# Kernel tuning notes

Measured on AMD Instinct MI355X. Metric: run time of the kernel, lower is better.

## Reference

```python
import jax, jax.numpy as jnp
import numpy as np

# config (matches init_kwargs)
D, H, KV, HD, L, F, V, NC, S = 1024, 16, 4, 64, 6, 4096, 4096, 15, 16
KVD = KV * HD            # 256
ATTN_SCALING = 1.0
EPS = 1e-6
POS = 7                  # current cache write position


def _rms(x, w):
    return x * jax.lax.rsqrt(jnp.mean(x * x, axis=-1, keepdims=True) + EPS) * w


def _rot(x):
    h = x.shape[-1] // 2
    return jnp.concatenate([-x[..., h:], x[..., :h]], axis=-1)


def setup_inputs() -> dict:
    key = jax.random.key(0)
    ks = iter(jax.random.split(key, 24))
    def rn(shape, s):
        return jax.random.normal(next(ks), shape, jnp.float32) * s
    return {
        "input_embeds": rn((1, D, 1, 1), 1.0),
        "cache_length": POS,
        "key_cache": rn((1, L * KVD, 1, S), 0.5),
        "key_padding_mask": jnp.where(jnp.arange(S) <= POS, 0.0, -1e9)[None, :].astype(jnp.float32),
        "kv_cache_update_mask": (jnp.arange(S) == POS).astype(jnp.float32)[None, :],
        "value_cache": rn((1, L * KVD, 1, S), 0.5),
        "inv_freq": 1.0 / (10000.0 ** (jnp.arange(0, HD, 2, dtype=jnp.float32) / HD)),
        "Wq": rn((L, H * HD, D), 0.02),
        "Wk": rn((L, KVD, D), 0.02),
        "Wv": rn((L, KVD, D), 0.02),
        "Wo": rn((L, D, H * HD), 0.02),
        "ln1_w": jnp.ones((L, D), jnp.float32),
        "ln2_w": jnp.ones((L, D), jnp.float32),
        "qn_w": jnp.ones((L, HD), jnp.float32),
        "kn_w": jnp.ones((L, HD), jnp.float32),
        "Wgate": rn((L, F, D), 0.02),
        "Wup": rn((L, F, D), 0.02),
        "Wdown": rn((L, D, F), 0.02),
        "norm_w": jnp.ones((D,), jnp.float32),
        "lm_head_w": rn((NC, V, D), 0.02),
    }


def _forward(input_embeds, key_cache, key_padding_mask, kv_cache_update_mask,
             value_cache, inv_freq, Wq, Wk, Wv, Wo, ln1_w, ln2_w, qn_w, kn_w,
             Wgate, Wup, Wdown, norm_w, lm_head_w, cache_length):
    pos = jnp.asarray(cache_length, jnp.float32)
    freqs = inv_freq * pos                       # [HD/2]
    emb = jnp.concatenate([freqs, freqs])        # [HD]
    cos = jnp.cos(emb) * ATTN_SCALING
    sin = jnp.sin(emb) * ATTN_SCALING
    umask = kv_cache_update_mask[0]              # [S]
    pmask = key_padding_mask[0]                  # [S]
    kcache = key_cache.reshape(L, KVD, S)
    vcache = value_cache.reshape(L, KVD, S)
    hidden0 = input_embeds.reshape(D)
    n_rep = H // KV
    scale = 1.0 / (HD ** 0.5)

    def layer(hidden, p):
        Wq_, Wk_, Wv_, Wo_, ln1, ln2, qn, kn, Wg_, Wu_, Wd_, kc_l, vc_l = p
        h = _rms(hidden, ln1)
        q = _rms((Wq_ @ h).reshape(H, HD), qn)   # [H,HD]
        k = _rms((Wk_ @ h).reshape(KV, HD), kn)  # [KV,HD]
        v = (Wv_ @ h).reshape(KV, HD)
        q = q * cos + _rot(q) * sin
        k = k * cos + _rot(k) * sin
        nk = k.reshape(KVD)
        nv = v.reshape(KVD)
        # masked scatter-write into this layer's cache slice
        kc = kc_l * (1.0 - umask) + nk[:, None] * umask   # [KVD,S]
        vc = vc_l * (1.0 - umask) + nv[:, None] * umask
        kc = jnp.repeat(kc.reshape(KV, HD, S), n_rep, axis=0)  # GQA expand -> [H,HD,S]
        vc = jnp.repeat(vc.reshape(KV, HD, S), n_rep, axis=0)
        scores = jnp.einsum('hd,hds->hs', q, kc) * scale + pmask  # [H,S]
        aw = jax.nn.softmax(scores, axis=-1)
        ao = jnp.einsum('hs,hds->hd', aw, vc).reshape(H * HD)
        hidden = hidden + Wo_ @ ao
        h = _rms(hidden, ln2)
        hidden = hidden + Wd_ @ (jax.nn.silu(Wg_ @ h) * (Wu_ @ h))
        return hidden, (nk, nv)

    hidden, (nks, nvs) = jax.lax.scan(
        layer, hidden0,
        (Wq, Wk, Wv, Wo, ln1_w, ln2_w, qn_w, kn_w, Wgate, Wup, Wdown, kcache, vcache))

    normed = _rms(hidden, norm_w)                          # [D]
    all_logits = jnp.einsum('nvd,d->nv', lm_head_w, normed)[None]  # [1,NC,V]
    hidden_out = normed.reshape(1, D, 1, 1)
    um4 = kv_cache_update_mask[:, None, None, :]           # [1,1,1,S]
    new_k = nks.reshape(1, L * KVD, 1, 1)
    new_v = nvs.reshape(1, L * KVD, 1, 1)
    nkc = key_cache * (1.0 - um4) + new_k * um4
    nvc = value_cache * (1.0 - um4) + new_v * um4
    return (all_logits, hidden_out, nkc, nvc)


def reference(input_embeds, cache_length, key_cache, key_padding_mask,
              kv_cache_update_mask, value_cache, inv_freq, Wq, Wk, Wv, Wo,
              ln1_w, ln2_w, qn_w, kn_w, Wgate, Wup, Wdown, norm_w, lm_head_w):
    return _forward(input_embeds, key_cache, key_padding_mask, kv_cache_update_mask,
                    value_cache, inv_freq, Wq, Wk, Wv, Wo, ln1_w, ln2_w, qn_w, kn_w,
                    Wgate, Wup, Wdown, norm_w, lm_head_w, cache_length)
```

## Files before the change

### kernel.cpp

```cpp
#include <hip/hip_runtime.h>

#define DD     1024
#define HH     16
#define KVH    4
#define HDIM   64
#define NLAYER 6
#define FDIM   4096
#define VDIM   4096
#define NCODE  15
#define SS     16
#define KVDIM  256
#define EPSF   1e-6f

__device__ __forceinline__ float dot4(float4 a, float4 b){
  return a.x*b.x + a.y*b.y + a.z*b.z + a.w*b.w;
}
__device__ __forceinline__ float wave_sum(float v){
  #pragma unroll
  for (int o=32;o;o>>=1) v += __shfl_xor(v,o);
  return v;
}
__device__ __forceinline__ float grp16_sum(float v){
  #pragma unroll
  for (int o=8;o;o>>=1) v += __shfl_xor(v,o);
  return v;
}
__device__ __forceinline__ float grp16_max(float v){
  #pragma unroll
  for (int o=8;o;o>>=1) v = fmaxf(v, __shfl_xor(v,o));
  return v;
}

__global__ __launch_bounds__(256) void k_init(const float* __restrict__ emb,
                                              float* __restrict__ hidden){
  ((float4*)hidden)[threadIdx.x] = ((const float4*)emb)[threadIdx.x];
}

__global__ __launch_bounds__(256) void k_qkv(
    const float* __restrict__ Wq, const float* __restrict__ Wk, const float* __restrict__ Wv,
    const float* __restrict__ hidden, const float* __restrict__ ln,
    float* __restrict__ out )
{
  __shared__ float xs[DD];
  __shared__ float red[4];
  const int t = threadIdx.x, lane = t & 63, wid = t >> 6;
  float4 hv = ((const float4*)hidden)[t];
  float ss = wave_sum(dot4(hv,hv));
  if (lane==0) red[wid] = ss;
  __syncthreads();
  const float inv = rsqrtf((red[0]+red[1]+red[2]+red[3])*(1.0f/DD) + EPSF);
  float4 lw = ((const float4*)ln)[t];
  float4 xv; xv.x=hv.x*inv*lw.x; xv.y=hv.y*inv*lw.y; xv.z=hv.z*inv*lw.z; xv.w=hv.w*inv*lw.w;
  ((float4*)xs)[t] = xv;
  __syncthreads();
  const int row = blockIdx.x*4 + wid;
  const float* Wrow;
  if (row < 1024)      Wrow = Wq + (size_t)row*DD;
  else if (row < 1280) Wrow = Wk + (size_t)(row-1024)*DD;
  else                 Wrow = Wv + (size_t)(row-1280)*DD;
  const float4* w4 = (const float4*)Wrow;
  const float4* x4 = (const float4*)xs;
  float acc = 0.f;
  #pragma unroll
  for (int j=0;j<4;j++) acc += dot4(w4[j*64+lane], x4[j*64+lane]);
  acc = wave_sum(acc);
  if (lane==0) out[row] = acc;
}

__global__ __launch_bounds__(256) void k_attn(
    const float* __restrict__ qbuf, const float* __restrict__ kbuf, const float* __restrict__ vbuf,
    const float* __restrict__ qn, const float* __restrict__ kn,
    const float* __restrict__ inv_freq, const int* __restrict__ cache_len,
    const float* __restrict__ kcache_l, const float* __restrict__ vcache_l,
    const float* __restrict__ pmask, const float* __restrict__ umask,
    float* __restrict__ ao, float* __restrict__ knew, float* __restrict__ vnew)
{
  __shared__ float qsh[DD];
  __shared__ float ksh[KVDIM];
  __shared__ float vsh[KVDIM];
  __shared__ float awsh[HH*SS];
  __shared__ float umsh[SS], pmsh[SS];
  const int t = threadIdx.x;
  if (t < SS){ umsh[t]=umask[t]; pmsh[t]=pmask[t]; }
  const float pos = (float)cache_len[0];

  {
    const int idx16 = t & 15;
    float4 q = ((const float4*)qbuf)[t];
    float ss = grp16_sum(dot4(q,q));
    const float inv = rsqrtf(ss*(1.0f/HDIM)+EPSF);
    float4 w = ((const float4*)qn)[idx16];
    float x0=q.x*inv*w.x, x1=q.y*inv*w.y, x2=q.z*inv*w.z, x3=q.w*inv*w.w;
    float p0=__shfl_xor(x0,8), p1=__shfl_xor(x1,8), p2=__shfl_xor(x2,8), p3=__shfl_xor(x3,8);
    const int d0 = idx16*4;
    const bool lolane = (idx16 < 8);
    const int m = lolane ? d0 : d0-32;
    const float f0=inv_freq[m]*pos, f1=inv_freq[m+1]*pos, f2=inv_freq[m+2]*pos, f3=inv_freq[m+3]*pos;
    const float sgn = lolane ? -1.f : 1.f;
    float4 r;
    r.x = x0*cosf(f0) + sgn*p0*sinf(f0);
    r.y = x1*cosf(f1) + sgn*p1*sinf(f1);
    r.z = x2*cosf(f2) + sgn*p2*sinf(f2);
    r.w = x3*cosf(f3) + sgn*p3*sinf(f3);
    ((float4*)qsh)[t] = r;
  }
  if (t < 64){
    const int idx16 = t & 15;
    float4 k = ((const float4*)kbuf)[t];
    float ss = grp16_sum(dot4(k,k));
    const float inv = rsqrtf(ss*(1.0f/HDIM)+EPSF);
    float4 w = ((const float4*)kn)[idx16];
    float x0=k.x*inv*w.x, x1=k.y*inv*w.y, x2=k.z*inv*w.z, x3=k.w*inv*w.w;
    float p0=__shfl_xor(x0,8), p1=__shfl_xor(x1,8), p2=__shfl_xor(x2,8), p3=__shfl_xor(x3,8);
    const int d0 = idx16*4;
    const bool lolane = (idx16 < 8);
    const int m = lolane ? d0 : d0-32;
    const float f0=inv_freq[m]*pos, f1=inv_freq[m+1]*pos, f2=inv_freq[m+2]*pos, f3=inv_freq[m+3]*pos;
    const float sgn = lolane ? -1.f : 1.f;
    float4 r;
    r.x = x0*cosf(f0) + sgn*p0*sinf(f0);
    r.y = x1*cosf(f1) + sgn*p1*sinf(f1);
    r.z = x2*cosf(f2) + sgn*p2*sinf(f2);
    r.w = x3*cosf(f3) + sgn*p3*sinf(f3);
    ((float4*)ksh)[t] = r;
    ((float4*)knew)[t] = r;
    float4 v = ((const float4*)vbuf)[t];
    ((float4*)vsh)[t] = v;
    ((float4*)vnew)[t] = v;
  }
  __syncthreads();
  {
    const int h = t>>4, s = t&15, kvh = h>>2;
    const float um = umsh[s], pm = pmsh[s];
    const float* kcol = kcache_l + (size_t)(kvh*HDIM)*SS + s;
    const float* ksrc = ksh + kvh*HDIM;
    const float* qv   = qsh + h*HDIM;
    float dot = 0.f;
    #pragma unroll
    for (int d=0; d<HDIM; d++){
      float kc = kcol[d*SS]*(1.f-um) + ksrc[d]*um;
      dot += qv[d]*kc;
    }
    const float sc = dot*0.125f + pm;
    const float mx = grp16_max(sc);
    const float e  = expf(sc-mx);
    const float sm = grp16_sum(e);
    awsh[t] = e/sm;
  }
  __syncthreads();
  {
    const int h = t>>4, idx16 = t&15, kvh = h>>2;
    const int cb = kvh*HDIM + idx16*4;
    float a0=0,a1=0,a2=0,a3=0;
    #pragma unroll
    for (int s=0;s<SS;s++){
      const float aw = awsh[h*16+s];
      const float um = umsh[s];
      a0 += aw*(vcache_l[(size_t)(cb+0)*SS+s]*(1.f-um)+vsh[cb+0]*um);
      a1 += aw*(vcache_l[(size_t)(cb+1)*SS+s]*(1.f-um)+vsh[cb+1]*um);
      a2 += aw*(vcache_l[(size_t)(cb+2)*SS+s]*(1.f-um)+vsh[cb+2]*um);
      a3 += aw*(vcache_l[(size_t)(cb+3)*SS+s]*(1.f-um)+vsh[cb+3]*um);
    }
    ((float4*)ao)[t] = make_float4(a0,a1,a2,a3);
  }
}

__global__ __launch_bounds__(256) void k_o(
    const float* __restrict__ Wo, const float* __restrict__ ao, float* __restrict__ hidden)
{
  __shared__ float xs[DD];
  const int t=threadIdx.x, lane=t&63, wid=t>>6;
  ((float4*)xs)[t] = ((const float4*)ao)[t];
  __syncthreads();
  const int row = blockIdx.x*4 + wid;
  const float4* w4 = (const float4*)(Wo + (size_t)row*DD);
  const float4* x4 = (const float4*)xs;
  float acc=0.f;
  #pragma unroll
  for (int j=0;j<4;j++) acc += dot4(w4[j*64+lane], x4[j*64+lane]);
  acc = wave_sum(acc);
  if (lane==0) hidden[row] += acc;
}

__global__ __launch_bounds__(256) void k_gu(
    const float* __restrict__ Wg, const float* __restrict__ Wu,
    const float* __restrict__ hidden, const float* __restrict__ ln,
    float* __restrict__ act)
{
  __shared__ float xs[DD];
  __shared__ float red[4];
  const int t=threadIdx.x, lane=t&63, wid=t>>6;
  float4 hv = ((const float4*)hidden)[t];
  float ss = wave_sum(dot4(hv,hv));
  if (lane==0) red[wid]=ss;
  __syncthreads();
  const float inv = rsqrtf((red[0]+red[1]+red[2]+red[3])*(1.0f/DD) + EPSF);
  float4 lw = ((const float4*)ln)[t];
  float4 xv; xv.x=hv.x*inv*lw.x; xv.y=hv.y*inv*lw.y; xv.z=hv.z*inv*lw.z; xv.w=hv.w*inv*lw.w;
  ((float4*)xs)[t] = xv;
  __syncthreads();
  const int row = blockIdx.x*4 + wid;
  const float4* g4 = (const float4*)(Wg + (size_t)row*DD);
  const float4* u4 = (const float4*)(Wu + (size_t)row*DD);
  const float4* x4 = (const float4*)xs;
  float ag=0.f, au=0.f;
  #pragma unroll
  for (int j=0;j<4;j++){
    float4 x = x4[j*64+lane];
    ag += dot4(g4[j*64+lane], x);
    au += dot4(u4[j*64+lane], x);
  }
  ag = wave_sum(ag); au = wave_sum(au);
  if (lane==0){
    float sg = ag/(1.f+expf(-ag));
    act[row] = sg*au;
  }
}

__global__ __launch_bounds__(256) void k_down(
    const float* __restrict__ Wd, const float* __restrict__ act, float* __restrict__ hidden)
{
  __shared__ float xs[FDIM];
  const int t=threadIdx.x, lane=t&63, wid=t>>6;
  #pragma unroll
  for (int j=0;j<4;j++) ((float4*)xs)[j*256+t] = ((const float4*)act)[j*256+t];
  __syncthreads();
  const int row = blockIdx.x*4 + wid;
  const float4* w4 = (const float4*)(Wd + (size_t)row*FDIM);
  const float4* x4 = (const float4*)xs;
  float acc=0.f;
  #pragma unroll
  for (int j=0;j<16;j++) acc += dot4(w4[j*64+lane], x4[j*64+lane]);
  acc = wave_sum(acc);
  if (lane==0) hidden[row] += acc;
}

__global__ __launch_bounds__(256) void k_finalize(
    const float* __restrict__ hidden, const float* __restrict__ norm_w,
    const float* __restrict__ kcache, const float* __restrict__ vcache,
    const float* __restrict__ knew, const float* __restrict__ vnew,
    const float* __restrict__ umask,
    float* __restrict__ normed, float* __restrict__ out_hidden,
    float* __restrict__ out_nkc, float* __restrict__ out_nvc)
{
  if (blockIdx.x == 0){
    __shared__ float red[4];
    const int t=threadIdx.x, lane=t&63, wid=t>>6;
    float4 hv = ((const float4*)hidden)[t];
    float ss = wave_sum(dot4(hv,hv));
    if (lane==0) red[wid]=ss;
    __syncthreads();
    const float inv = rsqrtf((red[0]+red[1]+red[2]+red[3])*(1.0f/DD) + EPSF);
    float4 w = ((const float4*)norm_w)[t];
    float4 nv; nv.x=hv.x*inv*w.x; nv.y=hv.y*inv*w.y; nv.z=hv.z*inv*w.z; nv.w=hv.w*inv*w.w;
    ((float4*)normed)[t]   = nv;
    ((float4*)out_hidden)[t] = nv;
  } else {
    const int j = (blockIdx.x-1)*256 + threadIdx.x;
    if (j < NLAYER*KVDIM*SS){
      const int s = j & 15, c = j >> 4;
      const float um = umask[s];
      out_nkc[j] = kcache[j]*(1.f-um) + knew[c]*um;
    } else {
      const int i = j - NLAYER*KVDIM*SS;
      const int s = i & 15, c = i >> 4;
      const float um = umask[s];
      out_nvc[i] = vcache[i]*(1.f-um) + vnew[c]*um;
    }
  }
}

__global__ __launch_bounds__(256) void k_lmhead(
    const float* __restrict__ W, const float* __restrict__ normed, float* __restrict__ out)
{
  __shared__ float xs[DD];
  const int t=threadIdx.x, lane=t&63, wid=t>>6;
  ((float4*)xs)[t] = ((const float4*)normed)[t];
  __syncthreads();
  const int row = blockIdx.x*4 + wid;
  const float4* w4 = (const float4*)(W + (size_t)row*DD);
  const float4* x4 = (const float4*)xs;
  float acc=0.f;
  #pragma unroll
  for (int j=0;j<4;j++) acc += dot4(w4[j*64+lane], x4[j*64+lane]);
  acc = wave_sum(acc);
  if (lane==0) out[row] = acc;
}

extern "C" void kernel_launch(void* const* d_in, const int* in_sizes, int n_in,
                              void* d_out, int out_size, void* d_ws, size_t ws_size,
                              hipStream_t stream)
{
  const float* emb    = (const float*)d_in[0];
  const int*   clen   = (const int*)  d_in[1];
  const float* kcache = (const float*)d_in[2];
  const float* pmask  = (const float*)d_in[3];
  const float* umask  = (const float*)d_in[4];
  const float* vcache = (const float*)d_in[5];
  const float* invf   = (const float*)d_in[6];
  const float* Wq     = (const float*)d_in[7];
  const float* Wk     = (const float*)d_in[8];
  const float* Wv     = (const float*)d_in[9];
  const float* Wo     = (const float*)d_in[10];
  const float* ln1    = (const float*)d_in[11];
  const float* ln2    = (const float*)d_in[12];
  const float* qn     = (const float*)d_in[13];
  const float* kn     = (const float*)d_in[14];
  const float* Wg     = (const float*)d_in[15];
  const float* Wu     = (const float*)d_in[16];
  const float* Wd     = (const float*)d_in[17];
  const float* nw     = (const float*)d_in[18];
  const float* lmw    = (const float*)d_in[19];
  float* out = (float*)d_out;
  float* ws  = (float*)d_ws;

  float* hidden = ws;
  float* qkv    = ws + 1024;
  float* ao     = ws + 2560;
  float* act    = ws + 3584;
  float* knew   = ws + 7680;
  float* vnew   = ws + 9216;
  float* normed = ws + 10752;

  float* out_logits = out;
  float* out_hidden = out + NCODE*VDIM;
  float* out_nkc    = out_hidden + DD;
  float* out_nvc    = out_nkc + NLAYER*KVDIM*SS;

  k_init<<<1,256,0,stream>>>(emb, hidden);
  for (int l=0; l<NLAYER; l++){
    k_qkv<<<384,256,0,stream>>>(Wq + (size_t)l*HH*HDIM*DD, Wk + (size_t)l*KVDIM*DD,
                                Wv + (size_t)l*KVDIM*DD, hidden, ln1 + l*DD, qkv);
    k_attn<<<1,256,0,stream>>>(qkv, qkv+1024, qkv+1280, qn + l*HDIM, kn + l*HDIM,
                               invf, clen,
                               kcache + (size_t)l*KVDIM*SS, vcache + (size_t)l*KVDIM*SS,
                               pmask, umask, ao, knew + l*KVDIM, vnew + l*KVDIM);
    k_o<<<256,256,0,stream>>>(Wo + (size_t)l*DD*HH*HDIM, ao, hidden);
    k_gu<<<1024,256,0,stream>>>(Wg + (size_t)l*FDIM*DD, Wu + (size_t)l*FDIM*DD,
                                hidden, ln2 + l*DD, act);
    k_down<<<256,256,0,stream>>>(Wd + (size_t)l*DD*FDIM, act, hidden);
  }
  k_finalize<<<193,256,0,stream>>>(hidden, nw, kcache, vcache, knew, vnew, umask,
                                   normed, out_hidden, out_nkc, out_nvc);
  k_lmhead<<<15360,256,0,stream>>>(lmw, normed, out_logits);
}
```

Baseline: 678.7 us.

## Fuse whole decode step into one persistent kernel with grid barriers

Replaces the roughly 32 separate kernel launches (qkv, attention, o-proj, gate/up, down per layer, plus finalize and lm head) with a single persistent 256-block kernel. A software grid barrier built on atomics separates the phases. The tiny attention step is computed redundantly in every block, which removes the single-block attention launch and the separate ao buffer. Cos/sin are precomputed once, and the gate/up, down and lm-head loops load several weight rows per wave to raise memory-level parallelism. The risks are barrier spin cost, the requirement that all 256 blocks be co-resident, and running the bandwidth-bound lm head with fewer blocks.

```diff
diff --git a/kernel.cpp b/kernel.cpp
--- a/kernel.cpp
+++ b/kernel.cpp
@@ -11,6 +11,7 @@
 #define SS     16
 #define KVDIM  256
 #define EPSF   1e-6f
+#define NBLK   256
 
 __device__ __forceinline__ float dot4(float4 a, float4 b){
   return a.x*b.x + a.y*b.y + a.z*b.z + a.w*b.w;
@@ -31,260 +32,298 @@
   return v;
 }
 
-__global__ __launch_bounds__(256) void k_init(const float* __restrict__ emb,
-                                              float* __restrict__ hidden){
-  ((float4*)hidden)[threadIdx.x] = ((const float4*)emb)[threadIdx.x];
-}
-
-__global__ __launch_bounds__(256) void k_qkv(
-    const float* __restrict__ Wq, const float* __restrict__ Wk, const float* __restrict__ Wv,
-    const float* __restrict__ hidden, const float* __restrict__ ln,
-    float* __restrict__ out )
+__device__ __forceinline__ void gbar(unsigned* bar){
+  __syncthreads();
+  if (threadIdx.x == 0){
+    __threadfence();
+    unsigned g = __hip_atomic_load(bar+1, __ATOMIC_RELAXED, __HIP_MEMORY_SCOPE_AGENT);
+    unsigned a = __hip_atomic_fetch_add(bar, 1u, __ATOMIC_RELAXED, __HIP_MEMORY_SCOPE_AGENT);
+    if (a == (unsigned)(NBLK-1)){
+      __hip_atomic_store(bar, 0u, __ATOMIC_RELAXED, __HIP_MEMORY_SCOPE_AGENT);
+      __hip_atomic_fetch_add(bar+1, 1u, __ATOMIC_RELEASE, __HIP_MEMORY_SCOPE_AGENT);
+    } else {
+      while (__hip_atomic_load(bar+1, __ATOMIC_RELAXED, __HIP_MEMORY_SCOPE_AGENT) == g)
+        __builtin_amdgcn_s_sleep(2);
+    }
+    __threadfence();
+  }
+  __syncthreads();
+}
+
+__global__ void k_barinit(unsigned* bar){ bar[0]=0u; bar[1]=0u; }
+
+__device__ __forceinline__ float4 rms_rope16(float4 x, const float4* nw4,
+                                             const float* cosb, const float* sinb,
+                                             int idx16)
 {
-  __shared__ float xs[DD];
-  __shared__ float red[4];
+  float ssum = grp16_sum(dot4(x,x));
+  const float inv = rsqrtf(ssum*(1.0f/HDIM)+EPSF);
+  float4 w = nw4[idx16];
+  float x0=x.x*inv*w.x, x1=x.y*inv*w.y, x2=x.z*inv*w.z, x3=x.w*inv*w.w;
+  float p0=__shfl_xor(x0,8), p1=__shfl_xor(x1,8), p2=__shfl_xor(x2,8), p3=__shfl_xor(x3,8);
+  float4 c = ((const float4*)cosb)[idx16];
+  float4 s = ((const float4*)sinb)[idx16];
+  const float sgn = (idx16 < 8) ? -1.f : 1.f;
+  float4 r;
+  r.x = x0*c.x + sgn*p0*s.x;
+  r.y = x1*c.y + sgn*p1*s.y;
+  r.z = x2*c.z + sgn*p2*s.z;
+  r.w = x3*c.w + sgn*p3*s.w;
+  return r;
+}
+
+__global__ __launch_bounds__(256) void k_fused(
+    const float* __restrict__ emb,   const int* __restrict__ clen,
+    const float* __restrict__ kcache,const float* __restrict__ pmask,
+    const float* __restrict__ umask, const float* __restrict__ vcache,
+    const float* __restrict__ invf,
+    const float* __restrict__ Wq,    const float* __restrict__ Wk,
+    const float* __restrict__ Wv,    const float* __restrict__ Wo,
+    const float* __restrict__ ln1,   const float* __restrict__ ln2,
+    const float* __restrict__ qn,    const float* __restrict__ kn,
+    const float* __restrict__ Wg,    const float* __restrict__ Wu,
+    const float* __restrict__ Wd,    const float* __restrict__ nw,
+    const float* __restrict__ lmw,
+    float* __restrict__ out_logits,  float* __restrict__ out_hidden,
+    float* __restrict__ out_nkc,     float* __restrict__ out_nvc,
+    float* __restrict__ ws,          unsigned* __restrict__ bar)
+{
   const int t = threadIdx.x, lane = t & 63, wid = t >> 6;
-  float4 hv = ((const float4*)hidden)[t];
-  float ss = wave_sum(dot4(hv,hv));
-  if (lane==0) red[wid] = ss;
-  __syncthreads();
-  const float inv = rsqrtf((red[0]+red[1]+red[2]+red[3])*(1.0f/DD) + EPSF);
-  float4 lw = ((const float4*)ln)[t];
-  float4 xv; xv.x=hv.x*inv*lw.x; xv.y=hv.y*inv*lw.y; xv.z=hv.z*inv*lw.z; xv.w=hv.w*inv*lw.w;
-  ((float4*)xs)[t] = xv;
-  __syncthreads();
-  const int row = blockIdx.x*4 + wid;
-  const float* Wrow;
-  if (row < 1024)      Wrow = Wq + (size_t)row*DD;
-  else if (row < 1280) Wrow = Wk + (size_t)(row-1024)*DD;
-  else                 Wrow = Wv + (size_t)(row-1280)*DD;
-  const float4* w4 = (const float4*)Wrow;
-  const float4* x4 = (const float4*)xs;
-  float acc = 0.f;
-  #pragma unroll
-  for (int j=0;j<4;j++) acc += dot4(w4[j*64+lane], x4[j*64+lane]);
-  acc = wave_sum(acc);
-  if (lane==0) out[row] = acc;
-}
-
-__global__ __launch_bounds__(256) void k_attn(
-    const float* __restrict__ qbuf, const float* __restrict__ kbuf, const float* __restrict__ vbuf,
-    const float* __restrict__ qn, const float* __restrict__ kn,
-    const float* __restrict__ inv_freq, const int* __restrict__ cache_len,
-    const float* __restrict__ kcache_l, const float* __restrict__ vcache_l,
-    const float* __restrict__ pmask, const float* __restrict__ umask,
-    float* __restrict__ ao, float* __restrict__ knew, float* __restrict__ vnew)
-{
-  __shared__ float qsh[DD];
-  __shared__ float ksh[KVDIM];
-  __shared__ float vsh[KVDIM];
+  const int gw = blockIdx.x*4 + wid;
+
+  __shared__ float xs[FDIM];
+  __shared__ float ksh[KVDIM], vsh[KVDIM];
   __shared__ float awsh[HH*SS];
   __shared__ float umsh[SS], pmsh[SS];
-  const int t = threadIdx.x;
-  if (t < SS){ umsh[t]=umask[t]; pmsh[t]=pmask[t]; }
-  const float pos = (float)cache_len[0];
+  __shared__ float red[4];
+
+  float* hidden = ws;
+  float* qkv    = ws + 1024;
+  float* act    = ws + 2560;
+  float* knew   = ws + 6656;
+  float* vnew   = ws + 8192;
+  float* cosb   = ws + 9728;
+  float* sinb   = ws + 9792;
+
+  if (t < SS){ umsh[t] = umask[t]; pmsh[t] = pmask[t]; }
+
+  if (blockIdx.x == 0){
+    ((float4*)hidden)[t] = ((const float4*)emb)[t];
+    if (t < 64){
+      const float f = invf[t & 31] * (float)clen[0];
+      cosb[t] = cosf(f);
+      sinb[t] = sinf(f);
+    }
+  }
+  gbar(bar);
+
+  for (int l = 0; l < NLAYER; ++l){
+    const float* Wq_l = Wq + (size_t)l*HH*HDIM*DD;
+    const float* Wk_l = Wk + (size_t)l*KVDIM*DD;
+    const float* Wv_l = Wv + (size_t)l*KVDIM*DD;
+    const float* Wo_l = Wo + (size_t)l*DD*HH*HDIM;
+    const float* Wg_l = Wg + (size_t)l*FDIM*DD;
+    const float* Wu_l = Wu + (size_t)l*FDIM*DD;
+    const float* Wd_l = Wd + (size_t)l*DD*FDIM;
+    const float* kc_l = kcache + (size_t)l*KVDIM*SS;
+    const float* vc_l = vcache + (size_t)l*KVDIM*SS;
+
+    {
+      float4 hv = ((const float4*)hidden)[t];
+      float ssum = wave_sum(dot4(hv,hv));
+      if (lane==0) red[wid] = ssum;
+      __syncthreads();
+      const float inv = rsqrtf((red[0]+red[1]+red[2]+red[3])*(1.0f/DD) + EPSF);
+      float4 lw = ((const float4*)(ln1 + l*DD))[t];
+      float4 xv; xv.x=hv.x*inv*lw.x; xv.y=hv.y*inv*lw.y; xv.z=hv.z*inv*lw.z; xv.w=hv.w*inv*lw.w;
+      ((float4*)xs)[t] = xv;
+      __syncthreads();
+      const float4* x4 = (const float4*)xs;
+      const float4* wa = (const float4*)(Wq_l + (size_t)gw*DD);
+      if (gw < 512){
+        const float* Wrow = (gw < 256) ? (Wk_l + (size_t)gw*DD) : (Wv_l + (size_t)(gw-256)*DD);
+        const float4* wb = (const float4*)Wrow;
+        float4 a0=wa[lane], a1=wa[64+lane], a2=wa[128+lane], a3=wa[192+lane];
+        float4 b0=wb[lane], b1=wb[64+lane], b2=wb[128+lane], b3=wb[192+lane];
+        float accA = dot4(a0,x4[lane])+dot4(a1,x4[64+lane])+dot4(a2,x4[128+lane])+dot4(a3,x4[192+lane]);
+        float accB = dot4(b0,x4[lane])+dot4(b1,x4[64+lane])+dot4(b2,x4[128+lane])+dot4(b3,x4[192+lane]);
+        accA = wave_sum(accA); accB = wave_sum(accB);
+        if (lane==0){ qkv[gw] = accA; qkv[1024+gw] = accB; }
+      } else {
+        float4 a0=wa[lane], a1=wa[64+lane], a2=wa[128+lane], a3=wa[192+lane];
+        float accA = dot4(a0,x4[lane])+dot4(a1,x4[64+lane])+dot4(a2,x4[128+lane])+dot4(a3,x4[192+lane]);
+        accA = wave_sum(accA);
+        if (lane==0) qkv[gw] = accA;
+      }
+    }
+    gbar(bar);
+
+    {
+      const int idx16 = t & 15;
+      {
+        float4 q = ((const float4*)qkv)[t];
+        float4 r = rms_rope16(q, (const float4*)(qn + l*HDIM), cosb, sinb, idx16);
+        ((float4*)xs)[t] = r;
+      }
+      if (t < 64){
+        float4 k = ((const float4*)(qkv+1024))[t];
+        float4 r = rms_rope16(k, (const float4*)(kn + l*HDIM), cosb, sinb, idx16);
+        ((float4*)ksh)[t] = r;
+        float4 v = ((const float4*)(qkv+1280))[t];
+        ((float4*)vsh)[t] = v;
+        if (blockIdx.x == 0){
+          ((float4*)(knew + l*KVDIM))[t] = r;
+          ((float4*)(vnew + l*KVDIM))[t] = v;
+        }
+      }
+      __syncthreads();
+      {
+        const int h = t>>4, s = t&15, kvh = h>>2;
+        const float um = umsh[s], pm = pmsh[s];
+        const float* kcol = kc_l + (size_t)(kvh*HDIM)*SS + s;
+        const float* ksrc = ksh + kvh*HDIM;
+        const float* qv   = xs + h*HDIM;
+        float dot = 0.f;
+        #pragma unroll
+        for (int d=0; d<HDIM; d++){
+          float kc = kcol[d*SS]*(1.f-um) + ksrc[d]*um;
+          dot += qv[d]*kc;
+        }
+        const float sc = dot*0.125f + pm;
+        const float mx = grp16_max(sc);
+        const float e  = expf(sc-mx);
+        const float sm = grp16_sum(e);
+        awsh[t] = e/sm;
+      }
+      __syncthreads();
+      {
+        const int h = t>>4, i16 = t&15, kvh = h>>2;
+        const int cb = kvh*HDIM + i16*4;
+        float a0=0,a1=0,a2=0,a3=0;
+        #pragma unroll
+        for (int s=0;s<SS;s++){
+          const float aw = awsh[h*16+s];
+          const float um = umsh[s];
+          a0 += aw*(vc_l[(size_t)(cb+0)*SS+s]*(1.f-um)+vsh[cb+0]*um);
+          a1 += aw*(vc_l[(size_t)(cb+1)*SS+s]*(1.f-um)+vsh[cb+1]*um);
+          a2 += aw*(vc_l[(size_t)(cb+2)*SS+s]*(1.f-um)+vsh[cb+2]*um);
+          a3 += aw*(vc_l[(size_t)(cb+3)*SS+s]*(1.f-um)+vsh[cb+3]*um);
+        }
+        ((float4*)(xs+1024))[t] = make_float4(a0,a1,a2,a3);
+      }
+      __syncthreads();
+      {
+        const float4* w4 = (const float4*)(Wo_l + (size_t)gw*DD);
+        const float4* x4 = (const float4*)(xs+1024);
+        float4 w0=w4[lane], w1=w4[64+lane], w2=w4[128+lane], w3=w4[192+lane];
+        float acc = dot4(w0,x4[lane])+dot4(w1,x4[64+lane])+dot4(w2,x4[128+lane])+dot4(w3,x4[192+lane]);
+        acc = wave_sum(acc);
+        if (lane==0) hidden[gw] += acc;
+      }
+    }
+    gbar(bar);
+
+    {
+      float4 hv = ((const float4*)hidden)[t];
+      float ssum = wave_sum(dot4(hv,hv));
+      if (lane==0) red[wid] = ssum;
+      __syncthreads();
+      const float inv = rsqrtf((red[0]+red[1]+red[2]+red[3])*(1.0f/DD) + EPSF);
+      float4 lw = ((const float4*)(ln2 + l*DD))[t];
+      float4 xv; xv.x=hv.x*inv*lw.x; xv.y=hv.y*inv*lw.y; xv.z=hv.z*inv*lw.z; xv.w=hv.w*inv*lw.w;
+      ((float4*)xs)[t] = xv;
+      __syncthreads();
+      const float4* x4 = (const float4*)xs;
+      #pragma unroll
+      for (int half=0; half<2; half++){
+        const int r0 = gw + half*2048;
+        const int r1 = r0 + 1024;
+        const float4* g0 = (const float4*)(Wg_l + (size_t)r0*DD);
+        const float4* u0 = (const float4*)(Wu_l + (size_t)r0*DD);
+        const float4* g1 = (const float4*)(Wg_l + (size_t)r1*DD);
+        const float4* u1 = (const float4*)(Wu_l + (size_t)r1*DD);
+        float4 wg0[4], wu0[4], wg1[4], wu1[4];
+        #pragma unroll
+        for (int j=0;j<4;j++){
+          wg0[j]=g0[j*64+lane]; wu0[j]=u0[j*64+lane];
+          wg1[j]=g1[j*64+lane]; wu1[j]=u1[j*64+lane];
+        }
+        float ag0=0,au0=0,ag1=0,au1=0;
+        #pragma unroll
+        for (int j=0;j<4;j++){
+          float4 x = x4[j*64+lane];
+          ag0+=dot4(wg0[j],x); au0+=dot4(wu0[j],x);
+          ag1+=dot4(wg1[j],x); au1+=dot4(wu1[j],x);
+        }
+        ag0=wave_sum(ag0); au0=wave_sum(au0); ag1=wave_sum(ag1); au1=wave_sum(au1);
+        if (lane==0){
+          act[r0] = ag0/(1.f+expf(-ag0))*au0;
+          act[r1] = ag1/(1.f+expf(-ag1))*au1;
+        }
+      }
+    }
+    gbar(bar);
+
+    {
+      #pragma unroll
+      for (int j=0;j<4;j++) ((float4*)xs)[j*256+t] = ((const float4*)act)[j*256+t];
+      __syncthreads();
+      const float4* w4 = (const float4*)(Wd_l + (size_t)gw*FDIM);
+      const float4* x4 = (const float4*)xs;
+      float4 wv[16];
+      #pragma unroll
+      for (int j=0;j<16;j++) wv[j] = w4[j*64+lane];
+      float acc = 0.f;
+      #pragma unroll
+      for (int j=0;j<16;j++) acc += dot4(wv[j], x4[j*64+lane]);
+      acc = wave_sum(acc);
+      if (lane==0) hidden[gw] += acc;
+    }
+    gbar(bar);
+  }
 
   {
-    const int idx16 = t & 15;
-    float4 q = ((const float4*)qbuf)[t];
-    float ss = grp16_sum(dot4(q,q));
-    const float inv = rsqrtf(ss*(1.0f/HDIM)+EPSF);
-    float4 w = ((const float4*)qn)[idx16];
-    float x0=q.x*inv*w.x, x1=q.y*inv*w.y, x2=q.z*inv*w.z, x3=q.w*inv*w.w;
-    float p0=__shfl_xor(x0,8), p1=__shfl_xor(x1,8), p2=__shfl_xor(x2,8), p3=__shfl_xor(x3,8);
-    const int d0 = idx16*4;
-    const bool lolane = (idx16 < 8);
-    const int m = lolane ? d0 : d0-32;
-    const float f0=inv_freq[m]*pos, f1=inv_freq[m+1]*pos, f2=inv_freq[m+2]*pos, f3=inv_freq[m+3]*pos;
-    const float sgn = lolane ? -1.f : 1.f;
-    float4 r;
-    r.x = x0*cosf(f0) + sgn*p0*sinf(f0);
-    r.y = x1*cosf(f1) + sgn*p1*sinf(f1);
-    r.z = x2*cosf(f2) + sgn*p2*sinf(f2);
-    r.w = x3*cosf(f3) + sgn*p3*sinf(f3);
-    ((float4*)qsh)[t] = r;
-  }
-  if (t < 64){
-    const int idx16 = t & 15;
-    float4 k = ((const float4*)kbuf)[t];
-    float ss = grp16_sum(dot4(k,k));
-    const float inv = rsqrtf(ss*(1.0f/HDIM)+EPSF);
-    float4 w = ((const float4*)kn)[idx16];
-    float x0=k.x*inv*w.x, x1=k.y*inv*w.y, x2=k.z*inv*w.z, x3=k.w*inv*w.w;
-    float p0=__shfl_xor(x0,8), p1=__shfl_xor(x1,8), p2=__shfl_xor(x2,8), p3=__shfl_xor(x3,8);
-    const int d0 = idx16*4;
-    const bool lolane = (idx16 < 8);
-    const int m = lolane ? d0 : d0-32;
-    const float f0=inv_freq[m]*pos, f1=inv_freq[m+1]*pos, f2=inv_freq[m+2]*pos, f3=inv_freq[m+3]*pos;
-    const float sgn = lolane ? -1.f : 1.f;
-    float4 r;
-    r.x = x0*cosf(f0) + sgn*p0*sinf(f0);
-    r.y = x1*cosf(f1) + sgn*p1*sinf(f1);
-    r.z = x2*cosf(f2) + sgn*p2*sinf(f2);
-    r.w = x3*cosf(f3) + sgn*p3*sinf(f3);
-    ((float4*)ksh)[t] = r;
-    ((float4*)knew)[t] = r;
-    float4 v = ((const float4*)vbuf)[t];
-    ((float4*)vsh)[t] = v;
-    ((float4*)vnew)[t] = v;
-  }
-  __syncthreads();
-  {
-    const int h = t>>4, s = t&15, kvh = h>>2;
-    const float um = umsh[s], pm = pmsh[s];
-    const float* kcol = kcache_l + (size_t)(kvh*HDIM)*SS + s;
-    const float* ksrc = ksh + kvh*HDIM;
-    const float* qv   = qsh + h*HDIM;
-    float dot = 0.f;
-    #pragma unroll
-    for (int d=0; d<HDIM; d++){
-      float kc = kcol[d*SS]*(1.f-um) + ksrc[d]*um;
-      dot += qv[d]*kc;
-    }
-    const float sc = dot*0.125f + pm;
-    const float mx = grp16_max(sc);
-    const float e  = expf(sc-mx);
-    const float sm = grp16_sum(e);
-    awsh[t] = e/sm;
-  }
-  __syncthreads();
-  {
-    const int h = t>>4, idx16 = t&15, kvh = h>>2;
-    const int cb = kvh*HDIM + idx16*4;
-    float a0=0,a1=0,a2=0,a3=0;
-    #pragma unroll
-    for (int s=0;s<SS;s++){
-      const float aw = awsh[h*16+s];
-      const float um = umsh[s];
-      a0 += aw*(vcache_l[(size_t)(cb+0)*SS+s]*(1.f-um)+vsh[cb+0]*um);
-      a1 += aw*(vcache_l[(size_t)(cb+1)*SS+s]*(1.f-um)+vsh[cb+1]*um);
-      a2 += aw*(vcache_l[(size_t)(cb+2)*SS+s]*(1.f-um)+vsh[cb+2]*um);
-      a3 += aw*(vcache_l[(size_t)(cb+3)*SS+s]*(1.f-um)+vsh[cb+3]*um);
-    }
-    ((float4*)ao)[t] = make_float4(a0,a1,a2,a3);
-  }
-}
-
-__global__ __launch_bounds__(256) void k_o(
-    const float* __restrict__ Wo, const float* __restrict__ ao, float* __restrict__ hidden)
-{
-  __shared__ float xs[DD];
-  const int t=threadIdx.x, lane=t&63, wid=t>>6;
-  ((float4*)xs)[t] = ((const float4*)ao)[t];
-  __syncthreads();
-  const int row = blockIdx.x*4 + wid;
-  const float4* w4 = (const float4*)(Wo + (size_t)row*DD);
-  const float4* x4 = (const float4*)xs;
-  float acc=0.f;
-  #pragma unroll
-  for (int j=0;j<4;j++) acc += dot4(w4[j*64+lane], x4[j*64+lane]);
-  acc = wave_sum(acc);
-  if (lane==0) hidden[row] += acc;
-}
-
-__global__ __launch_bounds__(256) void k_gu(
-    const float* __restrict__ Wg, const float* __restrict__ Wu,
-    const float* __restrict__ hidden, const float* __restrict__ ln,
-    float* __restrict__ act)
-{
-  __shared__ float xs[DD];
-  __shared__ float red[4];
-  const int t=threadIdx.x, lane=t&63, wid=t>>6;
-  float4 hv = ((const float4*)hidden)[t];
-  float ss = wave_sum(dot4(hv,hv));
-  if (lane==0) red[wid]=ss;
-  __syncthreads();
-  const float inv = rsqrtf((red[0]+red[1]+red[2]+red[3])*(1.0f/DD) + EPSF);
-  float4 lw = ((const float4*)ln)[t];
-  float4 xv; xv.x=hv.x*inv*lw.x; xv.y=hv.y*inv*lw.y; xv.z=hv.z*inv*lw.z; xv.w=hv.w*inv*lw.w;
-  ((float4*)xs)[t] = xv;
-  __syncthreads();
-  const int row = blockIdx.x*4 + wid;
-  const float4* g4 = (const float4*)(Wg + (size_t)row*DD);
-  const float4* u4 = (const float4*)(Wu + (size_t)row*DD);
-  const float4* x4 = (const float4*)xs;
-  float ag=0.f, au=0.f;
-  #pragma unroll
-  for (int j=0;j<4;j++){
-    float4 x = x4[j*64+lane];
-    ag += dot4(g4[j*64+lane], x);
-    au += dot4(u4[j*64+lane], x);
-  }
-  ag = wave_sum(ag); au = wave_sum(au);
-  if (lane==0){
-    float sg = ag/(1.f+expf(-ag));
-    act[row] = sg*au;
-  }
-}
-
-__global__ __launch_bounds__(256) void k_down(
-    const float* __restrict__ Wd, const float* __restrict__ act, float* __restrict__ hidden)
-{
-  __shared__ float xs[FDIM];
-  const int t=threadIdx.x, lane=t&63, wid=t>>6;
-  #pragma unroll
-  for (int j=0;j<4;j++) ((float4*)xs)[j*256+t] = ((const float4*)act)[j*256+t];
-  __syncthreads();
-  const int row = blockIdx.x*4 + wid;
-  const float4* w4 = (const float4*)(Wd + (size_t)row*FDIM);
-  const float4* x4 = (const float4*)xs;
-  float acc=0.f;
-  #pragma unroll
-  for (int j=0;j<16;j++) acc += dot4(w4[j*64+lane], x4[j*64+lane]);
-  acc = wave_sum(acc);
-  if (lane==0) hidden[row] += acc;
-}
-
-__global__ __launch_bounds__(256) void k_finalize(
-    const float* __restrict__ hidden, const float* __restrict__ norm_w,
-    const float* __restrict__ kcache, const float* __restrict__ vcache,
-    const float* __restrict__ knew, const float* __restrict__ vnew,
-    const float* __restrict__ umask,
-    float* __restrict__ normed, float* __restrict__ out_hidden,
-    float* __restrict__ out_nkc, float* __restrict__ out_nvc)
-{
-  if (blockIdx.x == 0){
-    __shared__ float red[4];
-    const int t=threadIdx.x, lane=t&63, wid=t>>6;
     float4 hv = ((const float4*)hidden)[t];
-    float ss = wave_sum(dot4(hv,hv));
-    if (lane==0) red[wid]=ss;
+    float ssum = wave_sum(dot4(hv,hv));
+    if (lane==0) red[wid] = ssum;
     __syncthreads();
     const float inv = rsqrtf((red[0]+red[1]+red[2]+red[3])*(1.0f/DD) + EPSF);
-    float4 w = ((const float4*)norm_w)[t];
+    float4 w = ((const float4*)nw)[t];
     float4 nv; nv.x=hv.x*inv*w.x; nv.y=hv.y*inv*w.y; nv.z=hv.z*inv*w.z; nv.w=hv.w*inv*w.w;
-    ((float4*)normed)[t]   = nv;
-    ((float4*)out_hidden)[t] = nv;
-  } else {
-    const int j = (blockIdx.x-1)*256 + threadIdx.x;
-    if (j < NLAYER*KVDIM*SS){
+    ((float4*)xs)[t] = nv;
+    if (blockIdx.x == 0) ((float4*)out_hidden)[t] = nv;
+    __syncthreads();
+    const float4* x4 = (const float4*)xs;
+    for (int it=0; it<15; ++it){
+      const int r0 = it*4096 + gw;
+      const float4* p0 = (const float4*)(lmw + (size_t)r0*DD);
+      const float4* p1 = (const float4*)(lmw + (size_t)(r0+1024)*DD);
+      const float4* p2 = (const float4*)(lmw + (size_t)(r0+2048)*DD);
+      const float4* p3 = (const float4*)(lmw + (size_t)(r0+3072)*DD);
+      float4 w0[4],w1[4],w2[4],w3[4];
+      #pragma unroll
+      for (int j=0;j<4;j++){ w0[j]=p0[j*64+lane]; w1[j]=p1[j*64+lane]; w2[j]=p2[j*64+lane]; w3[j]=p3[j*64+lane]; }
+      float a0=0,a1=0,a2=0,a3=0;
+      #pragma unroll
+      for (int j=0;j<4;j++){
+        float4 x = x4[j*64+lane];
+        a0+=dot4(w0[j],x); a1+=dot4(w1[j],x); a2+=dot4(w2[j],x); a3+=dot4(w3[j],x);
+      }
+      a0=wave_sum(a0); a1=wave_sum(a1); a2=wave_sum(a2); a3=wave_sum(a3);
+      if (lane==0){
+        out_logits[r0]      = a0;
+        out_logits[r0+1024] = a1;
+        out_logits[r0+2048] = a2;
+        out_logits[r0+3072] = a3;
+      }
+    }
+    for (int j = blockIdx.x*256 + t; j < NLAYER*KVDIM*SS; j += NBLK*256){
       const int s = j & 15, c = j >> 4;
-      const float um = umask[s];
+      const float um = umsh[s];
       out_nkc[j] = kcache[j]*(1.f-um) + knew[c]*um;
-    } else {
-      const int i = j - NLAYER*KVDIM*SS;
-      const int s = i & 15, c = i >> 4;
-      const float um = umask[s];
-      out_nvc[i] = vcache[i]*(1.f-um) + vnew[c]*um;
+      out_nvc[j] = vcache[j]*(1.f-um) + vnew[c]*um;
     }
   }
-}
-
-__global__ __launch_bounds__(256) void k_lmhead(
-    const float* __restrict__ W, const float* __restrict__ normed, float* __restrict__ out)
-{
-  __shared__ float xs[DD];
-  const int t=threadIdx.x, lane=t&63, wid=t>>6;
-  ((float4*)xs)[t] = ((const float4*)normed)[t];
-  __syncthreads();
-  const int row = blockIdx.x*4 + wid;
-  const float4* w4 = (const float4*)(W + (size_t)row*DD);
-  const float4* x4 = (const float4*)xs;
-  float acc=0.f;
-  #pragma unroll
-  for (int j=0;j<4;j++) acc += dot4(w4[j*64+lane], x4[j*64+lane]);
-  acc = wave_sum(acc);
-  if (lane==0) out[row] = acc;
 }
 
 extern "C" void kernel_launch(void* const* d_in, const int* in_sizes, int n_in,
@@ -314,33 +353,15 @@
   float* out = (float*)d_out;
   float* ws  = (float*)d_ws;
 
-  float* hidden = ws;
-  float* qkv    = ws + 1024;
-  float* ao     = ws + 2560;
-  float* act    = ws + 3584;
-  float* knew   = ws + 7680;
-  float* vnew   = ws + 9216;
-  float* normed = ws + 10752;
-
   float* out_logits = out;
   float* out_hidden = out + NCODE*VDIM;
   float* out_nkc    = out_hidden + DD;
   float* out_nvc    = out_nkc + NLAYER*KVDIM*SS;
 
-  k_init<<<1,256,0,stream>>>(emb, hidden);
-  for (int l=0; l<NLAYER; l++){
-    k_qkv<<<384,256,0,stream>>>(Wq + (size_t)l*HH*HDIM*DD, Wk + (size_t)l*KVDIM*DD,
-                                Wv + (size_t)l*KVDIM*DD, hidden, ln1 + l*DD, qkv);
-    k_attn<<<1,256,0,stream>>>(qkv, qkv+1024, qkv+1280, qn + l*HDIM, kn + l*HDIM,
-                               invf, clen,
-                               kcache + (size_t)l*KVDIM*SS, vcache + (size_t)l*KVDIM*SS,
-                               pmask, umask, ao, knew + l*KVDIM, vnew + l*KVDIM);
-    k_o<<<256,256,0,stream>>>(Wo + (size_t)l*DD*HH*HDIM, ao, hidden);
-    k_gu<<<1024,256,0,stream>>>(Wg + (size_t)l*FDIM*DD, Wu + (size_t)l*FDIM*DD,
-                                hidden, ln2 + l*DD, act);
-    k_down<<<256,256,0,stream>>>(Wd + (size_t)l*DD*FDIM, act, hidden);
-  }
-  k_finalize<<<193,256,0,stream>>>(hidden, nw, kcache, vcache, knew, vnew, umask,
-                                   normed, out_hidden, out_nkc, out_nvc);
-  k_lmhead<<<15360,256,0,stream>>>(lmw, normed, out_logits);
-}
+  unsigned* bar = (unsigned*)(ws + 16384);
+
+  k_barinit<<<1,1,0,stream>>>(bar);
+  k_fused<<<NBLK,256,0,stream>>>(emb, clen, kcache, pmask, umask, vcache, invf,
+                                 Wq, Wk, Wv, Wo, ln1, ln2, qn, kn, Wg, Wu, Wd, nw, lmw,
+                                 out_logits, out_hidden, out_nkc, out_nvc, ws, bar);
+}
```

New measurement: 1.217 ms. 1.79x slower.
